# Kernel tuning notes

Measured on AMD Instinct MI355X. Metric: run time of the kernel, lower is better.

Reference implementation:

```python
import jax, jax.numpy as jnp
import numpy as np

T_OUT = 12  # num_timesteps_output


def setup_inputs() -> dict:
    key = jax.random.key(0)
    ks = jax.random.split(key, 12)
    B, N, T, F = 32, 325, 12, 2
    C, H = 10, 64
    s = 0.08  # weight init scale (~1/sqrt(H)) to keep gates in sane range
    return {
        "A": jnp.zeros((N, N), jnp.float32),
        "X": jax.random.normal(ks[0], (B, N, T, F), jnp.float32),
        "enc_Wih": jax.random.normal(ks[1], (C, 3 * H, F), jnp.float32) * s,
        "enc_Whh": jax.random.normal(ks[2], (C, 3 * H, H), jnp.float32) * s,
        "enc_bih": jax.random.normal(ks[3], (C, 3 * H), jnp.float32) * s,
        "enc_bhh": jax.random.normal(ks[4], (C, 3 * H), jnp.float32) * s,
        "dec_Wih": jax.random.normal(ks[5], (C, 3 * H, 1), jnp.float32) * s,
        "dec_Whh": jax.random.normal(ks[6], (C, 3 * H, H), jnp.float32) * s,
        "dec_bih": jax.random.normal(ks[7], (C, 3 * H), jnp.float32) * s,
        "dec_bhh": jax.random.normal(ks[8], (C, 3 * H), jnp.float32) * s,
        "lin_W": jax.random.normal(ks[9], (C, 1, H), jnp.float32) * s,
        "lin_b": jax.random.normal(ks[10], (C, 1), jnp.float32) * s,
        "embed": jax.random.normal(ks[11], (N, C), jnp.float32),
    }


def _gru_update(gi, gh, h, H):
    # PyTorch GRU gate order: r, z, n
    r = jax.nn.sigmoid(gi[..., :H] + gh[..., :H])
    z = jax.nn.sigmoid(gi[..., H:2 * H] + gh[..., H:2 * H])
    n = jnp.tanh(gi[..., 2 * H:] + r * gh[..., 2 * H:])
    return (1.0 - z) * n + z * h


def reference(A, X, enc_Wih, enc_Whh, enc_bih, enc_bhh,
              dec_Wih, dec_Whh, dec_bih, dec_bhh, lin_W, lin_b, embed):
    B, N, T, F = X.shape
    C = enc_Wih.shape[0]
    H = enc_Whh.shape[-1]
    BN = B * N

    # (T, BN, F): time-major, batch*nodes flattened (matches X.view(-1,T,F).permute(1,0,2))
    Xs = jnp.transpose(X.reshape(BN, T, F), (1, 0, 2))

    def enc_step(h, x_t):  # h: (C, BN, H), x_t: (BN, F)
        gi = jnp.einsum('bf,cgf->cbg', x_t, enc_Wih) + enc_bih[:, None, :]
        gh = jnp.einsum('cbh,cgh->cbg', h, enc_Whh) + enc_bhh[:, None, :]
        return _gru_update(gi, gh, h, H), None

    h0 = jnp.zeros((C, BN, H), X.dtype)
    h_enc, _ = jax.lax.scan(enc_step, h0, Xs)  # (C, BN, H)

    # initial decoder input: last observed value of feature 0
    lv0 = jnp.broadcast_to(Xs[-1, :, 0][None, :, None], (C, BN, 1))

    def dec_step(carry, _):
        h, lv = carry
        gi = jnp.einsum('cbf,cgf->cbg', lv, dec_Wih) + dec_bih[:, None, :]
        gh = jnp.einsum('cbh,cgh->cbg', h, dec_Whh) + dec_bhh[:, None, :]
        h = _gru_update(gi, gh, h, H)
        value = jnp.einsum('cbh,coh->cbo', h, lin_W) + lin_b[:, None, :]  # (C, BN, 1)
        # original does last_value = value.detach()
        return (h, jax.lax.stop_gradient(value)), value

    (_, _), vals = jax.lax.scan(dec_step, (h_enc, lv0), None, length=T_OUT)
    # vals: (T_out, C, BN, 1) -> (B, N, T_out, C)
    out = jnp.transpose(vals[..., 0], (2, 0, 1)).reshape(B, N, T_OUT, C)

    weight = jax.nn.softmax(embed, axis=-1)  # (N, C)
    return jnp.einsum('bntc,nc->bnt', out, weight)
```

## Files before the change

### kernel.cpp

```cpp
#include <hip/hip_runtime.h>
#include <math.h>

#define N_   325
#define BN_  10400
#define R_   32

typedef _Float16 h8v __attribute__((ext_vector_type(8)));
typedef float    f4v __attribute__((ext_vector_type(4)));

#define L1C  1.4426950408889634f
#define L2C  2.8853900817779268f

__device__ __forceinline__ float rcp_f(float x){ return __builtin_amdgcn_rcpf(x); }
#if __has_builtin(__builtin_amdgcn_exp2f)
__device__ __forceinline__ float exp2_f(float x){ return __builtin_amdgcn_exp2f(x); }
#else
__device__ __forceinline__ float exp2_f(float x){ return __expf(x * 0.6931471805599453f); }
#endif

__device__ __forceinline__ int plane_idx(int m,int k){
    return m*64 + ((((k>>3)^(m&7))<<3)|(k&7));
}
__device__ __forceinline__ int frag_idx(int m,int kb){
    return m*64 + ((kb^(m&7))<<3);
}

__device__ __forceinline__ void load_B(const float* __restrict__ Whh, int jcol, int kg,
                                       h8v Bf[3][2])
{
#pragma unroll
    for (int g3=0; g3<3; ++g3)
#pragma unroll
        for (int ch=0; ch<2; ++ch) {
            const float* p = Whh + (g3*64 + jcol)*64 + ch*32 + kg*8;
            float4 a = *(const float4*)p;
            float4 b = *(const float4*)(p+4);
            h8v v;
            v[0]=(_Float16)a.x; v[1]=(_Float16)a.y; v[2]=(_Float16)a.z; v[3]=(_Float16)a.w;
            v[4]=(_Float16)b.x; v[5]=(_Float16)b.y; v[6]=(_Float16)b.z; v[7]=(_Float16)b.w;
            Bf[g3][ch] = v;
        }
}

__global__ void __launch_bounds__(256, 4) krnn_kernel(
    const float* __restrict__ X,
    const float* __restrict__ eWih, const float* __restrict__ eWhh,
    const float* __restrict__ ebih, const float* __restrict__ ebhh,
    const float* __restrict__ dWih, const float* __restrict__ dWhh,
    const float* __restrict__ dbih, const float* __restrict__ dbhh,
    const float* __restrict__ linW, const float* __restrict__ linb,
    const float* __restrict__ embed, float* __restrict__ out)
{
    __shared__ _Float16 sH[2][R_*64];
    __shared__ float2 sX2[12*R_];
    __shared__ float sWgt[R_];
    __shared__ float sVp[2][R_*4];

    const int c    = blockIdx.y;
    const int row0 = blockIdx.x * R_;
    const int tid  = threadIdx.x;
    const int lane = tid & 63;
    const int wv   = tid >> 6;
    const int nl   = lane & 15;
    const int kg   = lane >> 4;
    const int jcol = wv*16 + nl;

    for (int i = tid; i < 12*R_; i += 256) {
        int t = i >> 5, m = i & (R_-1);
        const float* p = X + (size_t)(row0+m)*24 + 2*t;
        sX2[i] = make_float2(p[0], p[1]);
    }
    if (tid < R_) {
        int n = (row0 + tid) % N_;
        float e[10], mx = -1e30f;
#pragma unroll
        for (int cc=0; cc<10; ++cc){ e[cc]=embed[n*10+cc]; mx=fmaxf(mx,e[cc]); }
        float den = 0.0f;
#pragma unroll
        for (int cc=0; cc<10; ++cc) den += exp2_f((e[cc]-mx)*L1C);
        sWgt[tid] = exp2_f((e[c]-mx)*L1C) * rcp_f(den);
    }

    h8v Bf[3][2];
    load_B(eWhh + c*12288, jcol, kg, Bf);

    float ew0_r, ew1_r, ew0_z, ew1_z;
    float ebss[2];
    float ew0n2, ew1n2, ebin2, ebh_n;
    {
        ew0_r = eWih[c*384 + jcol*2];       ew1_r = eWih[c*384 + jcol*2 + 1];
        ebss[0] = -L1C*(ebih[c*192 + jcol] + ebhh[c*192 + jcol]);
        int gc = 64 + jcol;
        ew0_z = eWih[c*384 + gc*2];         ew1_z = eWih[c*384 + gc*2 + 1];
        ebss[1] = -L1C*(ebih[c*192 + gc] + ebhh[c*192 + gc]);
        gc = 128 + jcol;
        ew0n2 = -L2C*eWih[c*384 + gc*2];    ew1n2 = -L2C*eWih[c*384 + gc*2 + 1];
        ebin2 = -L2C*ebih[c*192 + gc];
        ebh_n = ebhh[c*192 + gc];
    }
    h8v BeR, BeZ;
#pragma unroll
    for (int i=0;i<8;++i){ BeR[i]=(_Float16)0.0f; BeZ[i]=(_Float16)0.0f; }
    if (kg == 0) {
        BeR[0]=(_Float16)ew0_r; BeR[1]=(_Float16)ew1_r;
        BeZ[0]=(_Float16)ew0_z; BeZ[1]=(_Float16)ew1_z;
    }

    float hreg[2][4];
#pragma unroll
    for (int Mt=0;Mt<2;++Mt)
#pragma unroll
        for (int r4=0;r4<4;++r4) hreg[Mt][r4]=0.0f;

    __syncthreads();

#pragma unroll
    for (int Mt=0; Mt<2; ++Mt)
#pragma unroll
        for (int r4=0; r4<4; ++r4) {
            int m = Mt*16 + kg*4 + r4;
            float2 x = sX2[m];
            float r  = rcp_f(1.0f + exp2_f(fmaf(-L1C*ew0_r,x.x, fmaf(-L1C*ew1_r,x.y, ebss[0]))));
            float z  = rcp_f(1.0f + exp2_f(fmaf(-L1C*ew0_z,x.x, fmaf(-L1C*ew1_z,x.y, ebss[1]))));
            float gin2 = fmaf(ew0n2,x.x, fmaf(ew1n2,x.y, ebin2));
            float e  = exp2_f(fmaf(r*ebh_n, -L2C, gin2));
            float nn = fmaf(2.0f, rcp_f(1.0f + e), -1.0f);
            float hnew = nn - z*nn;
            hreg[Mt][r4] = hnew;
            sH[0][plane_idx(m,jcol)] = (_Float16)hnew;
        }
    __syncthreads();

    for (int t = 1; t < 12; ++t) {
        const int rp = (t+1)&1, wp = t&1;
        h8v Ah[2][2];
#pragma unroll
        for (int Mt=0; Mt<2; ++Mt)
#pragma unroll
            for (int ch=0; ch<2; ++ch)
                Ah[Mt][ch] = *(const h8v*)&sH[rp][frag_idx(Mt*16+nl, ch*4+kg)];

        h8v Ae[2];
#pragma unroll
        for (int Mt=0; Mt<2; ++Mt) {
#pragma unroll
            for (int i=0;i<8;++i) Ae[Mt][i] = (_Float16)0.0f;
            if (kg == 0) {
                float2 xe = sX2[t*R_ + Mt*16 + nl];
                Ae[Mt][0] = (_Float16)xe.x; Ae[Mt][1] = (_Float16)xe.y;
            }
        }

        f4v acc[2][3];
#pragma unroll
        for (int Mt=0;Mt<2;++Mt)
#pragma unroll
            for (int g3=0;g3<3;++g3)
#pragma unroll
                for (int r4=0;r4<4;++r4) acc[Mt][g3][r4]=0.0f;
#pragma unroll
        for (int Mt=0;Mt<2;++Mt) {
            acc[Mt][0] = __builtin_amdgcn_mfma_f32_16x16x32_f16(Ae[Mt], BeR, acc[Mt][0],0,0,0);
            acc[Mt][1] = __builtin_amdgcn_mfma_f32_16x16x32_f16(Ae[Mt], BeZ, acc[Mt][1],0,0,0);
#pragma unroll
            for (int g3=0;g3<3;++g3)
#pragma unroll
                for (int ch=0;ch<2;++ch)
                    acc[Mt][g3] = __builtin_amdgcn_mfma_f32_16x16x32_f16(Ah[Mt][ch], Bf[g3][ch], acc[Mt][g3],0,0,0);
        }

#pragma unroll
        for (int Mt=0;Mt<2;++Mt)
#pragma unroll
            for (int r4=0;r4<4;++r4) {
                int m = Mt*16 + kg*4 + r4;
                float2 x = sX2[t*R_ + m];
                float r  = rcp_f(1.0f + exp2_f(fmaf(acc[Mt][0][r4], -L1C, ebss[0])));
                float z  = rcp_f(1.0f + exp2_f(fmaf(acc[Mt][1][r4], -L1C, ebss[1])));
                float gin2 = fmaf(ew0n2,x.x, fmaf(ew1n2,x.y, ebin2));
                float q  = acc[Mt][2][r4] + ebh_n;
                float e  = exp2_f(fmaf(r*q, -L2C, gin2));
                float nn = fmaf(2.0f, rcp_f(1.0f + e), -1.0f);
                float hnew = nn + z*(hreg[Mt][r4] - nn);
                hreg[Mt][r4] = hnew;
                sH[wp][plane_idx(m,jcol)] = (_Float16)hnew;
            }
        __syncthreads();
    }

    load_B(dWhh + c*12288, jcol, kg, Bf);
    float dws[2], dbss[2], dwn2, dbin2, dbh_n;
    {
        int gc = jcol;
        dws[0]  = -L1C*dWih[c*192 + gc];
        dbss[0] = -L1C*(dbih[c*192 + gc] + dbhh[c*192 + gc]);
        gc = 64 + jcol;
        dws[1]  = -L1C*dWih[c*192 + gc];
        dbss[1] = -L1C*(dbih[c*192 + gc] + dbhh[c*192 + gc]);
        gc = 128 + jcol;
        dwn2  = -L2C*dWih[c*192 + gc];
        dbin2 = -L2C*dbih[c*192 + gc];
        dbh_n = dbhh[c*192 + gc];
    }
    const float lwl = linW[c*64 + jcol];
    const float lb  = linb[c];

    float vlv[2][4];
#pragma unroll
    for (int Mt=0;Mt<2;++Mt)
#pragma unroll
        for (int r4=0;r4<4;++r4)
            vlv[Mt][r4] = sX2[11*R_ + Mt*16 + kg*4 + r4].x;

    for (int s = 0; s < 12; ++s) {
        const int rp = (s+1)&1, wp = s&1;
        h8v Ah[2][2];
#pragma unroll
        for (int Mt=0; Mt<2; ++Mt)
#pragma unroll
            for (int ch=0; ch<2; ++ch)
                Ah[Mt][ch] = *(const h8v*)&sH[rp][frag_idx(Mt*16+nl, ch*4+kg)];

        f4v acc[2][3];
#pragma unroll
        for (int Mt=0;Mt<2;++Mt)
#pragma unroll
            for (int g3=0;g3<3;++g3)
#pragma unroll
                for (int r4=0;r4<4;++r4) acc[Mt][g3][r4]=0.0f;
#pragma unroll
        for (int Mt=0;Mt<2;++Mt)
#pragma unroll
            for (int g3=0;g3<3;++g3)
#pragma unroll
                for (int ch=0;ch<2;++ch)
                    acc[Mt][g3] = __builtin_amdgcn_mfma_f32_16x16x32_f16(Ah[Mt][ch], Bf[g3][ch], acc[Mt][g3],0,0,0);

#pragma unroll
        for (int Mt=0;Mt<2;++Mt)
#pragma unroll
            for (int r4=0;r4<4;++r4) {
                int m = Mt*16 + kg*4 + r4;
                float lv = vlv[Mt][r4];
                float r  = rcp_f(1.0f + exp2_f(fmaf(acc[Mt][0][r4], -L1C, fmaf(dws[0], lv, dbss[0]))));
                float z  = rcp_f(1.0f + exp2_f(fmaf(acc[Mt][1][r4], -L1C, fmaf(dws[1], lv, dbss[1]))));
                float q  = acc[Mt][2][r4] + dbh_n;
                float e  = exp2_f(fmaf(r*q, -L2C, fmaf(dwn2, lv, dbin2)));
                float nn = fmaf(2.0f, rcp_f(1.0f + e), -1.0f);
                float hnew = nn + z*(hreg[Mt][r4] - nn);
                hreg[Mt][r4] = hnew;
                sH[wp][plane_idx(m,jcol)] = (_Float16)hnew;

                float p = lwl * hnew;
                p += __shfl_xor(p, 1, 16);
                p += __shfl_xor(p, 2, 16);
                p += __shfl_xor(p, 4, 16);
                p += __shfl_xor(p, 8, 16);
                if (nl == 0) sVp[wp][m*4 + wv] = p;
            }
        __syncthreads();

#pragma unroll
        for (int Mt=0;Mt<2;++Mt)
#pragma unroll
            for (int r4=0;r4<4;++r4) {
                int m = Mt*16 + kg*4 + r4;
                float4 qv = *(const float4*)&sVp[wp][m*4];
                float v = (qv.x + qv.y) + (qv.z + qv.w) + lb;
                vlv[Mt][r4] = v;
                if (wv == 0 && nl == 0)
                    atomicAdd(&out[(size_t)(row0+m)*12 + s], sWgt[m]*v);
            }
    }
}

extern "C" void kernel_launch(void* const* d_in, const int* in_sizes, int n_in,
                              void* d_out, int out_size, void* d_ws, size_t ws_size,
                              hipStream_t stream) {
    const float* X    = (const float*)d_in[1];
    const float* eWih = (const float*)d_in[2];
    const float* eWhh = (const float*)d_in[3];
    const float* ebih = (const float*)d_in[4];
    const float* ebhh = (const float*)d_in[5];
    const float* dWih = (const float*)d_in[6];
    const float* dWhh = (const float*)d_in[7];
    const float* dbih = (const float*)d_in[8];
    const float* dbhh = (const float*)d_in[9];
    const float* linW = (const float*)d_in[10];
    const float* linb = (const float*)d_in[11];
    const float* emb  = (const float*)d_in[12];
    float* out = (float*)d_out;

    hipMemsetAsync(d_out, 0, (size_t)out_size * sizeof(float), stream);

    dim3 grid(BN_ / R_, 10);
    krnn_kernel<<<grid, dim3(256), 0, stream>>>(
        X, eWih, eWhh, ebih, ebhh, dWih, dWhh, dbih, dbhh, linW, linb, emb, out);
}
```

Before: 271.2 us.

## Fold gate scales and biases into MFMA operands; compute decoder output via MFMA

The -log2e and -2log2e gate scale factors are pre-multiplied into the fp16 recurrent weights. The encoder input weights and biases are folded into an augmented MFMA operand (a constant-1 column in A), which removes per-element FMAs and bias adds from the gate math. The separate t=0 encoder path is replaced by a zero-initialised hidden-state buffer. In the decoder, the shuffle-reduction plus extra sync used for the linear head is replaced by an MFMA against linW on the previous hidden state. This drops one barrier per step at the cost of extra MFMAs, fp16 rounding of biases and weights, and a trailing epilogue step.

```diff
diff --git a/kernel.cpp b/kernel.cpp
--- a/kernel.cpp
+++ b/kernel.cpp
@@ -25,9 +25,10 @@
     return m*64 + ((kb^(m&7))<<3);
 }
 
-__device__ __forceinline__ void load_B(const float* __restrict__ Whh, int jcol, int kg,
-                                       h8v Bf[3][2])
+__device__ __forceinline__ void load_B_scaled(const float* __restrict__ Whh,
+                                              int jcol, int kg, h8v Bf[3][2])
 {
+    const float sc[3] = { -L1C, -L1C, -L2C };
 #pragma unroll
     for (int g3=0; g3<3; ++g3)
 #pragma unroll
@@ -36,8 +37,10 @@
             float4 a = *(const float4*)p;
             float4 b = *(const float4*)(p+4);
             h8v v;
-            v[0]=(_Float16)a.x; v[1]=(_Float16)a.y; v[2]=(_Float16)a.z; v[3]=(_Float16)a.w;
-            v[4]=(_Float16)b.x; v[5]=(_Float16)b.y; v[6]=(_Float16)b.z; v[7]=(_Float16)b.w;
+            v[0]=(_Float16)(sc[g3]*a.x); v[1]=(_Float16)(sc[g3]*a.y);
+            v[2]=(_Float16)(sc[g3]*a.z); v[3]=(_Float16)(sc[g3]*a.w);
+            v[4]=(_Float16)(sc[g3]*b.x); v[5]=(_Float16)(sc[g3]*b.y);
+            v[6]=(_Float16)(sc[g3]*b.z); v[7]=(_Float16)(sc[g3]*b.w);
             Bf[g3][ch] = v;
         }
 }
@@ -54,7 +57,6 @@
     __shared__ _Float16 sH[2][R_*64];
     __shared__ float2 sX2[12*R_];
     __shared__ float sWgt[R_];
-    __shared__ float sVp[2][R_*4];
 
     const int c    = blockIdx.y;
     const int row0 = blockIdx.x * R_;
@@ -70,6 +72,7 @@
         const float* p = X + (size_t)(row0+m)*24 + 2*t;
         sX2[i] = make_float2(p[0], p[1]);
     }
+    for (int i = tid; i < R_*64; i += 256) sH[1][i] = (_Float16)0.0f;
     if (tid < R_) {
         int n = (row0 + tid) % N_;
         float e[10], mx = -1e30f;
@@ -82,29 +85,36 @@
     }
 
     h8v Bf[3][2];
-    load_B(eWhh + c*12288, jcol, kg, Bf);
-
-    float ew0_r, ew1_r, ew0_z, ew1_z;
-    float ebss[2];
-    float ew0n2, ew1n2, ebin2, ebh_n;
-    {
-        ew0_r = eWih[c*384 + jcol*2];       ew1_r = eWih[c*384 + jcol*2 + 1];
-        ebss[0] = -L1C*(ebih[c*192 + jcol] + ebhh[c*192 + jcol]);
-        int gc = 64 + jcol;
-        ew0_z = eWih[c*384 + gc*2];         ew1_z = eWih[c*384 + gc*2 + 1];
-        ebss[1] = -L1C*(ebih[c*192 + gc] + ebhh[c*192 + gc]);
+    load_B_scaled(eWhh + c*12288, jcol, kg, Bf);
+
+    h8v BeR, BeZ, BeN, BeN2;
+#pragma unroll
+    for (int i=0;i<8;++i){ BeR[i]=(_Float16)0.0f; BeZ[i]=(_Float16)0.0f;
+                           BeN[i]=(_Float16)0.0f; BeN2[i]=(_Float16)0.0f; }
+    if (kg == 0) {
+        int gc = jcol;
+        BeR[0]=(_Float16)(-L1C*eWih[c*384 + gc*2]);
+        BeR[1]=(_Float16)(-L1C*eWih[c*384 + gc*2 + 1]);
+        BeR[2]=(_Float16)(-L1C*(ebih[c*192+gc] + ebhh[c*192+gc]));
+        gc = 64 + jcol;
+        BeZ[0]=(_Float16)(-L1C*eWih[c*384 + gc*2]);
+        BeZ[1]=(_Float16)(-L1C*eWih[c*384 + gc*2 + 1]);
+        BeZ[2]=(_Float16)(-L1C*(ebih[c*192+gc] + ebhh[c*192+gc]));
         gc = 128 + jcol;
-        ew0n2 = -L2C*eWih[c*384 + gc*2];    ew1n2 = -L2C*eWih[c*384 + gc*2 + 1];
-        ebin2 = -L2C*ebih[c*192 + gc];
-        ebh_n = ebhh[c*192 + gc];
-    }
-    h8v BeR, BeZ;
-#pragma unroll
-    for (int i=0;i<8;++i){ BeR[i]=(_Float16)0.0f; BeZ[i]=(_Float16)0.0f; }
-    if (kg == 0) {
-        BeR[0]=(_Float16)ew0_r; BeR[1]=(_Float16)ew1_r;
-        BeZ[0]=(_Float16)ew0_z; BeZ[1]=(_Float16)ew1_z;
-    }
+        BeN[0]=(_Float16)(-L2C*eWih[c*384 + gc*2]);
+        BeN[1]=(_Float16)(-L2C*eWih[c*384 + gc*2 + 1]);
+        BeN[2]=(_Float16)(-L2C*ebih[c*192+gc]);
+        BeN2[2]=(_Float16)(-L2C*ebhh[c*192+gc]);
+    }
+    h8v Ae[2];
+#pragma unroll
+    for (int Mt=0;Mt<2;++Mt){
+#pragma unroll
+        for (int i=0;i<8;++i) Ae[Mt][i]=(_Float16)0.0f;
+        if (kg==0) Ae[Mt][2]=(_Float16)1.0f;
+    }
+
+    const f4v Z0 = {0.0f,0.0f,0.0f,0.0f};
 
     float hreg[2][4];
 #pragma unroll
@@ -114,24 +124,7 @@
 
     __syncthreads();
 
-#pragma unroll
-    for (int Mt=0; Mt<2; ++Mt)
-#pragma unroll
-        for (int r4=0; r4<4; ++r4) {
-            int m = Mt*16 + kg*4 + r4;
-            float2 x = sX2[m];
-            float r  = rcp_f(1.0f + exp2_f(fmaf(-L1C*ew0_r,x.x, fmaf(-L1C*ew1_r,x.y, ebss[0]))));
-            float z  = rcp_f(1.0f + exp2_f(fmaf(-L1C*ew0_z,x.x, fmaf(-L1C*ew1_z,x.y, ebss[1]))));
-            float gin2 = fmaf(ew0n2,x.x, fmaf(ew1n2,x.y, ebin2));
-            float e  = exp2_f(fmaf(r*ebh_n, -L2C, gin2));
-            float nn = fmaf(2.0f, rcp_f(1.0f + e), -1.0f);
-            float hnew = nn - z*nn;
-            hreg[Mt][r4] = hnew;
-            sH[0][plane_idx(m,jcol)] = (_Float16)hnew;
-        }
-    __syncthreads();
-
-    for (int t = 1; t < 12; ++t) {
+    for (int t = 0; t < 12; ++t) {
         const int rp = (t+1)&1, wp = t&1;
         h8v Ah[2][2];
 #pragma unroll
@@ -140,33 +133,27 @@
             for (int ch=0; ch<2; ++ch)
                 Ah[Mt][ch] = *(const h8v*)&sH[rp][frag_idx(Mt*16+nl, ch*4+kg)];
 
-        h8v Ae[2];
-#pragma unroll
-        for (int Mt=0; Mt<2; ++Mt) {
-#pragma unroll
-            for (int i=0;i<8;++i) Ae[Mt][i] = (_Float16)0.0f;
-            if (kg == 0) {
+        if (kg == 0) {
+#pragma unroll
+            for (int Mt=0; Mt<2; ++Mt) {
                 float2 xe = sX2[t*R_ + Mt*16 + nl];
                 Ae[Mt][0] = (_Float16)xe.x; Ae[Mt][1] = (_Float16)xe.y;
             }
         }
 
-        f4v acc[2][3];
-#pragma unroll
-        for (int Mt=0;Mt<2;++Mt)
-#pragma unroll
-            for (int g3=0;g3<3;++g3)
-#pragma unroll
-                for (int r4=0;r4<4;++r4) acc[Mt][g3][r4]=0.0f;
+        f4v a0[2], a1[2], a2[2], a3[2];
 #pragma unroll
         for (int Mt=0;Mt<2;++Mt) {
-            acc[Mt][0] = __builtin_amdgcn_mfma_f32_16x16x32_f16(Ae[Mt], BeR, acc[Mt][0],0,0,0);
-            acc[Mt][1] = __builtin_amdgcn_mfma_f32_16x16x32_f16(Ae[Mt], BeZ, acc[Mt][1],0,0,0);
-#pragma unroll
-            for (int g3=0;g3<3;++g3)
-#pragma unroll
-                for (int ch=0;ch<2;++ch)
-                    acc[Mt][g3] = __builtin_amdgcn_mfma_f32_16x16x32_f16(Ah[Mt][ch], Bf[g3][ch], acc[Mt][g3],0,0,0);
+            a0[Mt] = __builtin_amdgcn_mfma_f32_16x16x32_f16(Ae[Mt], BeR,  Z0, 0,0,0);
+            a1[Mt] = __builtin_amdgcn_mfma_f32_16x16x32_f16(Ae[Mt], BeZ,  Z0, 0,0,0);
+            a2[Mt] = __builtin_amdgcn_mfma_f32_16x16x32_f16(Ae[Mt], BeN2, Z0, 0,0,0);
+            a3[Mt] = __builtin_amdgcn_mfma_f32_16x16x32_f16(Ae[Mt], BeN,  Z0, 0,0,0);
+#pragma unroll
+            for (int ch=0; ch<2; ++ch) {
+                a0[Mt] = __builtin_amdgcn_mfma_f32_16x16x32_f16(Ah[Mt][ch], Bf[0][ch], a0[Mt],0,0,0);
+                a1[Mt] = __builtin_amdgcn_mfma_f32_16x16x32_f16(Ah[Mt][ch], Bf[1][ch], a1[Mt],0,0,0);
+                a2[Mt] = __builtin_amdgcn_mfma_f32_16x16x32_f16(Ah[Mt][ch], Bf[2][ch], a2[Mt],0,0,0);
+            }
         }
 
 #pragma unroll
@@ -174,12 +161,9 @@
 #pragma unroll
             for (int r4=0;r4<4;++r4) {
                 int m = Mt*16 + kg*4 + r4;
-                float2 x = sX2[t*R_ + m];
-                float r  = rcp_f(1.0f + exp2_f(fmaf(acc[Mt][0][r4], -L1C, ebss[0])));
-                float z  = rcp_f(1.0f + exp2_f(fmaf(acc[Mt][1][r4], -L1C, ebss[1])));
-                float gin2 = fmaf(ew0n2,x.x, fmaf(ew1n2,x.y, ebin2));
-                float q  = acc[Mt][2][r4] + ebh_n;
-                float e  = exp2_f(fmaf(r*q, -L2C, gin2));
+                float r  = rcp_f(1.0f + exp2_f(a0[Mt][r4]));
+                float z  = rcp_f(1.0f + exp2_f(a1[Mt][r4]));
+                float e  = exp2_f(fmaf(r, a2[Mt][r4], a3[Mt][r4]));
                 float nn = fmaf(2.0f, rcp_f(1.0f + e), -1.0f);
                 float hnew = nn + z*(hreg[Mt][r4] - nn);
                 hreg[Mt][r4] = hnew;
@@ -188,29 +172,39 @@
         __syncthreads();
     }
 
-    load_B(dWhh + c*12288, jcol, kg, Bf);
-    float dws[2], dbss[2], dwn2, dbin2, dbh_n;
+    load_B_scaled(dWhh + c*12288, jcol, kg, Bf);
+    h8v Blw[2];
+#pragma unroll
+    for (int ch=0; ch<2; ++ch) {
+        const float* p = linW + c*64 + ch*32 + kg*8;
+        float4 a = *(const float4*)p;
+        float4 b = *(const float4*)(p+4);
+        h8v v;
+        v[0]=(_Float16)a.x; v[1]=(_Float16)a.y; v[2]=(_Float16)a.z; v[3]=(_Float16)a.w;
+        v[4]=(_Float16)b.x; v[5]=(_Float16)b.y; v[6]=(_Float16)b.z; v[7]=(_Float16)b.w;
+        Blw[ch] = v;
+    }
+    float dws0, ks0, dws1, ks1, dwn2, kn, cbh2;
     {
         int gc = jcol;
-        dws[0]  = -L1C*dWih[c*192 + gc];
-        dbss[0] = -L1C*(dbih[c*192 + gc] + dbhh[c*192 + gc]);
+        dws0 = -L1C*dWih[c*192 + gc];
+        ks0  = -L1C*(dbih[c*192 + gc] + dbhh[c*192 + gc]);
         gc = 64 + jcol;
-        dws[1]  = -L1C*dWih[c*192 + gc];
-        dbss[1] = -L1C*(dbih[c*192 + gc] + dbhh[c*192 + gc]);
+        dws1 = -L1C*dWih[c*192 + gc];
+        ks1  = -L1C*(dbih[c*192 + gc] + dbhh[c*192 + gc]);
         gc = 128 + jcol;
-        dwn2  = -L2C*dWih[c*192 + gc];
-        dbin2 = -L2C*dbih[c*192 + gc];
-        dbh_n = dbhh[c*192 + gc];
-    }
-    const float lwl = linW[c*64 + jcol];
-    const float lb  = linb[c];
-
-    float vlv[2][4];
+        dwn2 = -L2C*dWih[c*192 + gc];
+        kn   = -L2C*dbih[c*192 + gc];
+        cbh2 = -L2C*dbhh[c*192 + gc];
+    }
+    const float lb = linb[c];
+
+    float lvx[2][4];
 #pragma unroll
     for (int Mt=0;Mt<2;++Mt)
 #pragma unroll
         for (int r4=0;r4<4;++r4)
-            vlv[Mt][r4] = sX2[11*R_ + Mt*16 + kg*4 + r4].x;
+            lvx[Mt][r4] = sX2[11*R_ + Mt*16 + kg*4 + r4].x;
 
     for (int s = 0; s < 12; ++s) {
         const int rp = (s+1)&1, wp = s&1;
@@ -221,56 +215,66 @@
             for (int ch=0; ch<2; ++ch)
                 Ah[Mt][ch] = *(const h8v*)&sH[rp][frag_idx(Mt*16+nl, ch*4+kg)];
 
-        f4v acc[2][3];
-#pragma unroll
-        for (int Mt=0;Mt<2;++Mt)
-#pragma unroll
-            for (int g3=0;g3<3;++g3)
-#pragma unroll
-                for (int r4=0;r4<4;++r4) acc[Mt][g3][r4]=0.0f;
-#pragma unroll
-        for (int Mt=0;Mt<2;++Mt)
-#pragma unroll
-            for (int g3=0;g3<3;++g3)
-#pragma unroll
-                for (int ch=0;ch<2;++ch)
-                    acc[Mt][g3] = __builtin_amdgcn_mfma_f32_16x16x32_f16(Ah[Mt][ch], Bf[g3][ch], acc[Mt][g3],0,0,0);
+        f4v a0[2], a1[2], a2[2], av[2];
+#pragma unroll
+        for (int Mt=0;Mt<2;++Mt) {
+            a0[Mt] = __builtin_amdgcn_mfma_f32_16x16x32_f16(Ah[Mt][0], Bf[0][0], Z0, 0,0,0);
+            a1[Mt] = __builtin_amdgcn_mfma_f32_16x16x32_f16(Ah[Mt][0], Bf[1][0], Z0, 0,0,0);
+            a2[Mt] = __builtin_amdgcn_mfma_f32_16x16x32_f16(Ah[Mt][0], Bf[2][0], Z0, 0,0,0);
+            a0[Mt] = __builtin_amdgcn_mfma_f32_16x16x32_f16(Ah[Mt][1], Bf[0][1], a0[Mt],0,0,0);
+            a1[Mt] = __builtin_amdgcn_mfma_f32_16x16x32_f16(Ah[Mt][1], Bf[1][1], a1[Mt],0,0,0);
+            a2[Mt] = __builtin_amdgcn_mfma_f32_16x16x32_f16(Ah[Mt][1], Bf[2][1], a2[Mt],0,0,0);
+        }
+        if (s > 0) {
+#pragma unroll
+            for (int Mt=0;Mt<2;++Mt) {
+                av[Mt] = __builtin_amdgcn_mfma_f32_16x16x32_f16(Ah[Mt][0], Blw[0], Z0, 0,0,0);
+                av[Mt] = __builtin_amdgcn_mfma_f32_16x16x32_f16(Ah[Mt][1], Blw[1], av[Mt],0,0,0);
+            }
+        }
 
 #pragma unroll
         for (int Mt=0;Mt<2;++Mt)
 #pragma unroll
             for (int r4=0;r4<4;++r4) {
                 int m = Mt*16 + kg*4 + r4;
-                float lv = vlv[Mt][r4];
-                float r  = rcp_f(1.0f + exp2_f(fmaf(acc[Mt][0][r4], -L1C, fmaf(dws[0], lv, dbss[0]))));
-                float z  = rcp_f(1.0f + exp2_f(fmaf(acc[Mt][1][r4], -L1C, fmaf(dws[1], lv, dbss[1]))));
-                float q  = acc[Mt][2][r4] + dbh_n;
-                float e  = exp2_f(fmaf(r*q, -L2C, fmaf(dwn2, lv, dbin2)));
+                float lv;
+                if (s == 0) lv = lvx[Mt][r4];
+                else {
+                    lv = av[Mt][r4] + lb;
+                    if (wv == 0 && nl == 0)
+                        atomicAdd(&out[(size_t)(row0+m)*12 + (s-1)], sWgt[m]*lv);
+                }
+                float r  = rcp_f(1.0f + exp2_f(a0[Mt][r4] + fmaf(dws0, lv, ks0)));
+                float z  = rcp_f(1.0f + exp2_f(a1[Mt][r4] + fmaf(dws1, lv, ks1)));
+                float e  = exp2_f(fmaf(r, a2[Mt][r4] + cbh2, fmaf(dwn2, lv, kn)));
                 float nn = fmaf(2.0f, rcp_f(1.0f + e), -1.0f);
                 float hnew = nn + z*(hreg[Mt][r4] - nn);
                 hreg[Mt][r4] = hnew;
                 sH[wp][plane_idx(m,jcol)] = (_Float16)hnew;
-
-                float p = lwl * hnew;
-                p += __shfl_xor(p, 1, 16);
-                p += __shfl_xor(p, 2, 16);
-                p += __shfl_xor(p, 4, 16);
-                p += __shfl_xor(p, 8, 16);
-                if (nl == 0) sVp[wp][m*4 + wv] = p;
             }
         __syncthreads();
-
-#pragma unroll
-        for (int Mt=0;Mt<2;++Mt)
-#pragma unroll
-            for (int r4=0;r4<4;++r4) {
-                int m = Mt*16 + kg*4 + r4;
-                float4 qv = *(const float4*)&sVp[wp][m*4];
-                float v = (qv.x + qv.y) + (qv.z + qv.w) + lb;
-                vlv[Mt][r4] = v;
-                if (wv == 0 && nl == 0)
-                    atomicAdd(&out[(size_t)(row0+m)*12 + s], sWgt[m]*v);
-            }
+    }
+
+    {
+        f4v av[2];
+#pragma unroll
+        for (int Mt=0; Mt<2; ++Mt) {
+            h8v A0 = *(const h8v*)&sH[1][frag_idx(Mt*16+nl, 0*4+kg)];
+            h8v A1 = *(const h8v*)&sH[1][frag_idx(Mt*16+nl, 1*4+kg)];
+            av[Mt] = __builtin_amdgcn_mfma_f32_16x16x32_f16(A0, Blw[0], Z0, 0,0,0);
+            av[Mt] = __builtin_amdgcn_mfma_f32_16x16x32_f16(A1, Blw[1], av[Mt],0,0,0);
+        }
+        if (wv == 0 && nl == 0) {
+#pragma unroll
+            for (int Mt=0;Mt<2;++Mt)
+#pragma unroll
+                for (int r4=0;r4<4;++r4) {
+                    int m = Mt*16 + kg*4 + r4;
+                    float v = av[Mt][r4] + lb;
+                    atomicAdd(&out[(size_t)(row0+m)*12 + 11], sWgt[m]*v);
+                }
+        }
     }
 }
 
```

Result: faster. 233.0 us (-14.1%).
